# Optimization experiments

Hardware: AMD Instinct MI355X
Metric: run time of the kernel (lower is better)

## Reference

```python
import jax, jax.numpy as jnp
import numpy as np

NUM_HEADS = 16
HIDDEN = 1024
HEAD_DIM = HIDDEN // NUM_HEADS


def setup_inputs() -> dict:
    key = jax.random.key(0)
    ks = jax.random.split(key, 9)
    B, S = 2, 2048
    s = 1.0 / np.sqrt(HIDDEN)
    return {
        "x": jax.random.normal(ks[0], (B, S, HIDDEN), dtype=jnp.float32),
        "Wq": jax.random.normal(ks[1], (HIDDEN, HIDDEN), dtype=jnp.float32) * s,
        "bq": jnp.zeros((HIDDEN,), dtype=jnp.float32),
        "Wk": jax.random.normal(ks[2], (HIDDEN, HIDDEN), dtype=jnp.float32) * s,
        "bk": jnp.zeros((HIDDEN,), dtype=jnp.float32),
        "Wv": jax.random.normal(ks[3], (HIDDEN, HIDDEN), dtype=jnp.float32) * s,
        "bv": jnp.zeros((HIDDEN,), dtype=jnp.float32),
        "Wo": jax.random.normal(ks[4], (HIDDEN, HIDDEN), dtype=jnp.float32) * s,
        "bo": jnp.zeros((HIDDEN,), dtype=jnp.float32),
    }


def reference(x, Wq, bq, Wk, bk, Wv, bv, Wo, bo):
    B, S, H = x.shape
    # project and split heads: [B, S, H] -> [B, nh, S, hd]
    def split_heads(t):
        return t.reshape(B, S, NUM_HEADS, HEAD_DIM).transpose(0, 2, 1, 3)

    q = split_heads(x @ Wq + bq)
    k = split_heads(x @ Wk + bk)
    v = split_heads(x @ Wv + bv)

    scores = jnp.einsum("bhqd,bhkd->bhqk", q, k) / jnp.sqrt(
        jnp.asarray(HEAD_DIM, dtype=x.dtype))
    probs = jax.nn.softmax(scores, axis=-1)
    # attn_drop_rate = 0.0 -> dropout is identity
    ctx = jnp.einsum("bhqk,bhkd->bhqd", probs, v)
    ctx = ctx.transpose(0, 2, 1, 3).reshape(B, S, H)
    out = ctx @ Wo + bo
    return out
```

## Files before the change

kernel.cpp:

```cpp
#include <hip/hip_runtime.h>

#define NHEADS 16
#define HDIM   64
#define SEQL   2048
#define HID    1024
#define NB     2
#define MT     4096

#define QSCALE 0.18033688011112042f

typedef float        f4_t   __attribute__((ext_vector_type(4)));
typedef float        f32x16 __attribute__((ext_vector_type(16)));
typedef unsigned int u32x4  __attribute__((ext_vector_type(4)));
typedef __bf16       bf16x8 __attribute__((ext_vector_type(8)));

typedef const __attribute__((address_space(1))) unsigned int* gas_ptr;
typedef __attribute__((address_space(3))) unsigned int*       las_ptr;

__device__ __forceinline__ void gload16(const void* g, void* l){
  __builtin_amdgcn_global_load_lds((gas_ptr)g, (las_ptr)l, 16, 0, 0);
}
__device__ __forceinline__ unsigned int pkbf(float a, float b){
  unsigned short lo = __builtin_bit_cast(unsigned short, (__bf16)a);
  unsigned short hi = __builtin_bit_cast(unsigned short, (__bf16)b);
  return (unsigned)lo | ((unsigned)hi << 16);
}
__device__ __forceinline__ unsigned short f2bf(float f){
  return __builtin_bit_cast(unsigned short, (__bf16)f);
}
__device__ __forceinline__ u32x4 ld16(const unsigned short* p){
  return *reinterpret_cast<const u32x4*>(p);
}
__device__ __forceinline__ f4_t mfma_bf16(u32x4 a, u32x4 b, f4_t c){
  return __builtin_amdgcn_mfma_f32_16x16x32_bf16(
      __builtin_bit_cast(bf16x8, a), __builtin_bit_cast(bf16x8, b), c, 0, 0, 0);
}
__device__ __forceinline__ f32x16 mfma32(u32x4 a, u32x4 b, f32x16 c){
  return __builtin_amdgcn_mfma_f32_32x32x16_bf16(
      __builtin_bit_cast(bf16x8, a), __builtin_bit_cast(bf16x8, b), c, 0, 0, 0);
}

#if __has_builtin(__builtin_amdgcn_permlane32_swap)
typedef unsigned int u32x2 __attribute__((ext_vector_type(2)));
__device__ __forceinline__ void plswap(unsigned int &a, unsigned int &b){
  u32x2 r = __builtin_amdgcn_permlane32_swap(a, b, false, false);
  a = r[0]; b = r[1];
}
#else
__device__ __forceinline__ void plswap(unsigned int &a, unsigned int &b){
  unsigned int as = (unsigned int)__shfl_xor((int)a, 32);
  unsigned int bs = (unsigned int)__shfl_xor((int)b, 32);
  bool hi = (threadIdx.x & 32) != 0;
  unsigned int na = hi ? bs : a;
  unsigned int nb = hi ? b  : as;
  a = na; b = nb;
}
#endif

__global__ __launch_bounds__(256) void xcast(const float* __restrict__ x,
                                             unsigned short* __restrict__ xb){
  int gid = blockIdx.x * 256 + threadIdx.x;
  float4 a = reinterpret_cast<const float4*>(x)[gid * 2];
  float4 b = reinterpret_cast<const float4*>(x)[gid * 2 + 1];
  u32x4 o;
  o[0] = pkbf(a.x, a.y);
  o[1] = pkbf(a.z, a.w);
  o[2] = pkbf(b.x, b.y);
  o[3] = pkbf(b.z, b.w);
  *reinterpret_cast<u32x4*>(&xb[gid * 8]) = o;
}

__global__ void prep_w(const float* __restrict__ Wq, const float* __restrict__ Wk,
                       const float* __restrict__ Wv, const float* __restrict__ Wo,
                       unsigned short* __restrict__ wqT, unsigned short* __restrict__ wkT,
                       unsigned short* __restrict__ wvT, unsigned short* __restrict__ woT){
  __shared__ float t[32][33];
  int z = blockIdx.z;
  const float* W = (z==0)?Wq:(z==1)?Wk:(z==2)?Wv:Wo;
  unsigned short* WT = (z==0)?wqT:(z==1)?wkT:(z==2)?wvT:woT;
  float sc = (z==0) ? QSCALE : 1.0f;
  int k0 = blockIdx.x*32, n0 = blockIdx.y*32;
  int tx = threadIdx.x, ty = threadIdx.y;
  #pragma unroll
  for (int ii=0; ii<4; ii++)
    t[ty+ii*8][tx] = W[(k0+ty+ii*8)*HID + n0+tx];
  __syncthreads();
  #pragma unroll
  for (int ii=0; ii<4; ii++)
    WT[(n0+ty+ii*8)*HID + k0+tx] = f2bf(t[tx][ty+ii*8] * sc);
}

__global__ __launch_bounds__(256) void qkv_gemm(
    const unsigned short* __restrict__ xb,
    const unsigned short* __restrict__ wqT, const unsigned short* __restrict__ wkT,
    const unsigned short* __restrict__ wvT,
    const float* __restrict__ bq, const float* __restrict__ bk, const float* __restrict__ bv,
    unsigned short* __restrict__ qo, unsigned short* __restrict__ ko,
    unsigned short* __restrict__ vto){
  __shared__ unsigned short As[2][128*32];
  __shared__ unsigned short Bs[2][128*32];
  const int z = blockIdx.z;
  const unsigned short* wT = (z==0)?wqT:(z==1)?wkT:wvT;
  const float* bias = (z==0)?bq:(z==1)?bk:bv;
  const float bscale = (z==0) ? QSCALE : 1.0f;
  const int m0 = blockIdx.x * 128;
  const int n0 = blockIdx.y * 128;
  const int tid = threadIdx.x;
  const int lane = tid & 63, w = tid >> 6;
  const int l15 = lane & 15, lg = lane >> 4;
  const int wr = (w >> 1) * 64, wc = (w & 1) * 64;
  const int srow = w*16 + (lane >> 2);
  const int skc  = (lane & 3) * 8;

  f4_t acc[4][4];
  f4_t z4 = {0.f, 0.f, 0.f, 0.f};
  #pragma unroll
  for (int i=0;i<4;i++)
    #pragma unroll
    for (int j=0;j<4;j++) acc[i][j] = z4;

  auto stageg = [&](int buf, int kt){
    #pragma unroll
    for (int c = 0; c < 2; c++) {
      int row = c*64 + srow;
      gload16(&xb[(m0+row)*HID + kt + skc], (char*)As[buf] + c*4096 + w*1024);
      gload16(&wT[(n0+row)*HID + kt + skc], (char*)Bs[buf] + c*4096 + w*1024);
    }
  };

  stageg(0, 0);
  int cur = 0;
  for (int kt = 0; kt < HID; kt += 32) {
    __syncthreads();
    if (kt + 32 < HID) stageg(cur^1, kt + 32);
    u32x4 a[4], b[4];
    #pragma unroll
    for (int i=0;i<4;i++) a[i] = ld16(&As[cur][(wr + i*16 + l15)*32 + lg*8]);
    #pragma unroll
    for (int j=0;j<4;j++) b[j] = ld16(&Bs[cur][(wc + j*16 + l15)*32 + lg*8]);
    __builtin_amdgcn_s_setprio(1);
    #pragma unroll
    for (int i=0;i<4;i++)
      #pragma unroll
      for (int j=0;j<4;j++)
        acc[i][j] = mfma_bf16(a[i], b[j], acc[i][j]);
    __builtin_amdgcn_s_setprio(0);
    cur ^= 1;
  }
  if (z == 2) {
    #pragma unroll
    for (int i=0;i<4;i++){
      int mrow = m0 + wr + i*16 + lg*4;
      int b_ = mrow >> 11, s = mrow & 2047;
      #pragma unroll
      for (int j=0;j<4;j++){
        int n = n0 + wc + j*16 + l15;
        float bs = bias[n];
        int h = n >> 6, d = n & 63;
        unsigned int lo = pkbf(acc[i][j][0]+bs, acc[i][j][1]+bs);
        unsigned int hi = pkbf(acc[i][j][2]+bs, acc[i][j][3]+bs);
        unsigned long long v8 = (unsigned long long)lo | ((unsigned long long)hi << 32);
        *reinterpret_cast<unsigned long long*>(
            vto + (((b_*NHEADS + h)*HDIM + d)*SEQL + s)) = v8;
      }
    }
  } else {
    unsigned short* outp = (z==0) ? qo : ko;
    #pragma unroll
    for (int i=0;i<4;i++){
      int mrow = m0 + wr + i*16 + lg*4;
      #pragma unroll
      for (int j=0;j<4;j++){
        int n = n0 + wc + j*16 + l15;
        float bs = bias[n] * bscale;
        int h = n >> 6, d = n & 63;
        #pragma unroll
        for (int r=0;r<4;r++){
          int m = mrow + r;
          int b_ = m >> 11, s = m & 2047;
          outp[(((b_*NHEADS + h)*SEQL) + s)*HDIM + d] = f2bf(acc[i][j][r] + bs);
        }
      }
    }
  }
}

__global__ __launch_bounds__(256, 4) void flash(
    const unsigned short* __restrict__ q,
    const unsigned short* __restrict__ k,
    const unsigned short* __restrict__ vT,
    float* __restrict__ po,
    float* __restrict__ pl,
    int kspan){
  __shared__ unsigned short Ks[2][4096];
  __shared__ unsigned short Vs[2][4096];
  const int bh = blockIdx.y;
  const int z = blockIdx.z;
  const int kb0 = z * kspan;
  const int tid = threadIdx.x;
  const int w = tid >> 6, lane = tid & 63;
  const int l31 = lane & 31, hi = lane >> 5;
  const int q0 = blockIdx.x*128 + w*32;
  const unsigned short* qb = q + (bh*SEQL + q0)*HDIM;
  const unsigned short* kp = k + bh*SEQL*HDIM;
  const unsigned short* vp = vT + bh*HDIM*SEQL;

  const int sr = w*16 + (lane >> 3);
  const int scol = ((lane & 7) ^ (sr & 7)) * 8;
  const int ldst = w*2048;

  u32x4 qf[4];
  #pragma unroll
  for (int c=0;c<4;c++)
    qf[c] = ld16(&qb[l31*HDIM + c*16 + hi*8]);

  u32x4 ones;
  ones[0] = 0x3F803F80u; ones[1] = 0x3F803F80u;
  ones[2] = 0x3F803F80u; ones[3] = 0x3F803F80u;

  f32x16 oacc[2], lsacc;
  f32x16 z16 = {0.f,0.f,0.f,0.f,0.f,0.f,0.f,0.f,0.f,0.f,0.f,0.f,0.f,0.f,0.f,0.f};
  oacc[0] = z16; oacc[1] = z16; lsacc = z16;

  auto stage = [&](int buf, int kb){
    const unsigned short* gk = kp + (kb + sr)*HDIM + scol;
    gload16(gk,          (char*)Ks[buf] + ldst);
    gload16(gk + 8*HDIM, (char*)Ks[buf] + ldst + 1024);
    const unsigned short* gv = vp + sr*SEQL + kb + scol;
    gload16(gv,          (char*)Vs[buf] + ldst);
    gload16(gv + 8*SEQL, (char*)Vs[buf] + ldst + 1024);
  };

  int cur = 0;
  stage(0, kb0);
  __syncthreads();

  const int rs = (l31 & 7) << 4;

  for (int kb = kb0; kb < kb0 + kspan; kb += 64) {
    if (kb + 64 < kb0 + kspan) stage(cur^1, kb + 64);
    const char* kbase = (const char*)Ks[cur];
    const char* vbase = (const char*)Vs[cur];

    f32x16 sacc[2];
    __builtin_amdgcn_s_setprio(1);
    #pragma unroll
    for (int t=0;t<2;t++){
      const char* rowb = kbase + (t*32 + l31)*128;
      #pragma unroll
      for (int c=0;c<4;c++){
        u32x4 kf = *reinterpret_cast<const u32x4*>(rowb + ((c*32 + hi*16) ^ rs));
        sacc[t] = (c==0) ? mfma32(kf, qf[0], z16) : mfma32(kf, qf[c], sacc[t]);
      }
    }
    __builtin_amdgcn_s_setprio(0);

    #pragma unroll
    for (int t=0;t<2;t++)
      #pragma unroll
      for (int r=0;r<16;r++) sacc[t][r] = exp2f(sacc[t][r]);

    u32x4 pa[4];
    #pragma unroll
    for (int t=0;t<2;t++)
      #pragma unroll
      for (int hf=0;hf<2;hf++){
        unsigned int c1 = pkbf(sacc[t][hf*8+0], sacc[t][hf*8+1]);
        unsigned int c2 = pkbf(sacc[t][hf*8+2], sacc[t][hf*8+3]);
        unsigned int c3 = pkbf(sacc[t][hf*8+4], sacc[t][hf*8+5]);
        unsigned int c4 = pkbf(sacc[t][hf*8+6], sacc[t][hf*8+7]);
        plswap(c1, c3);
        plswap(c2, c4);
        u32x4 f; f[0]=c1; f[1]=c2; f[2]=c3; f[3]=c4;
        pa[t*2+hf] = f;
      }

    __builtin_amdgcn_s_setprio(1);
    #pragma unroll
    for (int dt=0;dt<2;dt++){
      const char* rowb = vbase + (dt*32 + l31)*128;
      #pragma unroll
      for (int ks=0;ks<4;ks++){
        u32x4 vf = *reinterpret_cast<const u32x4*>(rowb + ((ks*32 + hi*16) ^ rs));
        oacc[dt] = mfma32(vf, pa[ks], oacc[dt]);
      }
    }
    #pragma unroll
    for (int ks=0;ks<4;ks++)
      lsacc = mfma32(ones, pa[ks], lsacc);
    __builtin_amdgcn_s_setprio(0);
    __syncthreads();
    cur ^= 1;
  }

  const int rowi = (z*NB*NHEADS + bh)*SEQL + q0 + l31;
  #pragma unroll
  for (int dt=0;dt<2;dt++){
    #pragma unroll
    for (int kq=0;kq<4;kq++){
      float4 o4;
      o4.x = oacc[dt][kq*4+0]; o4.y = oacc[dt][kq*4+1];
      o4.z = oacc[dt][kq*4+2]; o4.w = oacc[dt][kq*4+3];
      *reinterpret_cast<float4*>(po + rowi*HDIM + dt*32 + kq*8 + hi*4) = o4;
    }
  }
  if (hi == 0) pl[rowi] = lsacc[0];
}

__global__ __launch_bounds__(256) void combine(
    const float* __restrict__ po, const float* __restrict__ pl,
    unsigned short* __restrict__ ctx, int nsplit){
  int i = blockIdx.x*256 + threadIdx.x;
  int dq = i & 15;
  int rsi = i >> 4;
  int bh = rsi >> 11, s = rsi & 2047;
  int b_ = bh >> 4, h = bh & 15;
  float L = pl[rsi];
  float4 acc = reinterpret_cast<const float4*>(po)[rsi*16 + dq];
  for (int sp = 1; sp < nsplit; sp++) {
    float4 o1 = reinterpret_cast<const float4*>(po)[rsi*16 + dq + sp*NB*NHEADS*SEQL*16];
    L += pl[rsi + sp*NB*NHEADS*SEQL];
    acc.x += o1.x; acc.y += o1.y; acc.z += o1.z; acc.w += o1.w;
  }
  float inv = 1.0f / L;
  unsigned int lo = pkbf(acc.x*inv, acc.y*inv);
  unsigned int hv = pkbf(acc.z*inv, acc.w*inv);
  unsigned long long v8 = (unsigned long long)lo | ((unsigned long long)hv << 32);
  *reinterpret_cast<unsigned long long*>(
      ctx + (b_*SEQL + s)*HID + h*HDIM + dq*4) = v8;
}

__global__ __launch_bounds__(256) void out_gemm(
    const unsigned short* __restrict__ cb,
    const unsigned short* __restrict__ woT,
    const float* __restrict__ bo,
    float* __restrict__ out){
  __shared__ unsigned short As[2][128*32];
  __shared__ unsigned short Bs[2][128*32];
  const int m0 = blockIdx.x * 128;
  const int n0 = blockIdx.y * 128;
  const int tid = threadIdx.x;
  const int lane = tid & 63, w = tid >> 6;
  const int l15 = lane & 15, lg = lane >> 4;
  const int wr = (w >> 1) * 64, wc = (w & 1) * 64;
  const int srow = w*16 + (lane >> 2);
  const int skc  = (lane & 3) * 8;

  f4_t acc[4][4];
  f4_t z4 = {0.f,0.f,0.f,0.f};
  #pragma unroll
  for (int i=0;i<4;i++)
    #pragma unroll
    for (int j=0;j<4;j++) acc[i][j] = z4;

  auto stageg = [&](int buf, int kt){
    #pragma unroll
    for (int c = 0; c < 2; c++) {
      int row = c*64 + srow;
      gload16(&cb[(m0+row)*HID + kt + skc],  (char*)As[buf] + c*4096 + w*1024);
      gload16(&woT[(n0+row)*HID + kt + skc], (char*)Bs[buf] + c*4096 + w*1024);
    }
  };

  stageg(0, 0);
  int cur = 0;
  for (int kt = 0; kt < HID; kt += 32) {
    __syncthreads();
    if (kt + 32 < HID) stageg(cur^1, kt + 32);
    u32x4 a[4], b[4];
    #pragma unroll
    for (int i=0;i<4;i++) a[i] = ld16(&As[cur][(wr + i*16 + l15)*32 + lg*8]);
    #pragma unroll
    for (int j=0;j<4;j++) b[j] = ld16(&Bs[cur][(wc + j*16 + l15)*32 + lg*8]);
    __builtin_amdgcn_s_setprio(1);
    #pragma unroll
    for (int i=0;i<4;i++)
      #pragma unroll
      for (int j=0;j<4;j++)
        acc[i][j] = mfma_bf16(a[i], b[j], acc[i][j]);
    __builtin_amdgcn_s_setprio(0);
    cur ^= 1;
  }
  #pragma unroll
  for (int i=0;i<4;i++){
    int mrow = m0 + wr + i*16 + lg*4;
    #pragma unroll
    for (int j=0;j<4;j++){
      int n = n0 + wc + j*16 + l15;
      float bs = bo[n];
      #pragma unroll
      for (int r=0;r<4;r++)
        out[(mrow + r)*HID + n] = acc[i][j][r] + bs;
    }
  }
}

extern "C" void kernel_launch(void* const* d_in, const int* in_sizes, int n_in,
                              void* d_out, int out_size, void* d_ws, size_t ws_size,
                              hipStream_t stream){
  const float* x  = (const float*)d_in[0];
  const float* Wq = (const float*)d_in[1];
  const float* bq = (const float*)d_in[2];
  const float* Wk = (const float*)d_in[3];
  const float* bk = (const float*)d_in[4];
  const float* Wv = (const float*)d_in[5];
  const float* bv = (const float*)d_in[6];
  const float* Wo = (const float*)d_in[7];
  const float* bo = (const float*)d_in[8];
  float* out = (float*)d_out;

  char* ws = (char*)d_ws;
  size_t off = 0;
  auto alloc = [&](size_t bytes) -> void* {
    void* p = ws + off;
    off += (bytes + 255) & ~(size_t)255;
    return p;
  };
  unsigned short* xb   = (unsigned short*)alloc((size_t)MT*HID*2);
  unsigned short* wqT  = (unsigned short*)alloc((size_t)HID*HID*2);
  unsigned short* wkT  = (unsigned short*)alloc((size_t)HID*HID*2);
  unsigned short* wvT  = (unsigned short*)alloc((size_t)HID*HID*2);
  unsigned short* woT  = (unsigned short*)alloc((size_t)HID*HID*2);
  unsigned short* q_ws = (unsigned short*)alloc((size_t)MT*HID*2);
  unsigned short* k_ws = (unsigned short*)alloc((size_t)MT*HID*2);
  unsigned short* vT_ws= (unsigned short*)alloc((size_t)MT*HID*2);
  unsigned short* c_ws = (unsigned short*)alloc((size_t)MT*HID*2);
  size_t base_off = off;

  int nsplit = 1;
  {
    size_t need4 = base_off + (((size_t)4*MT*HID*4 + 255) & ~(size_t)255)
                            + (((size_t)4*NB*NHEADS*SEQL*4 + 255) & ~(size_t)255);
    size_t need2 = base_off + (((size_t)2*MT*HID*4 + 255) & ~(size_t)255)
                            + (((size_t)2*NB*NHEADS*SEQL*4 + 255) & ~(size_t)255);
    if (ws_size >= need4) nsplit = 4;
    else if (ws_size >= need2) nsplit = 2;
  }
  float* po = (float*)alloc((size_t)nsplit*MT*HID*4);
  float* pl = (float*)alloc((size_t)nsplit*NB*NHEADS*SEQL*4);
  int kspan = SEQL / nsplit;

  prep_w<<<dim3(32,32,4), dim3(32,8), 0, stream>>>(Wq,Wk,Wv,Wo, wqT,wkT,wvT,woT);
  xcast<<<dim3(2048), dim3(256), 0, stream>>>(x, xb);
  qkv_gemm<<<dim3(32,8,3), dim3(256), 0, stream>>>(xb, wqT,wkT,wvT, bq,bk,bv,
                                                   q_ws, k_ws, vT_ws);
  flash<<<dim3(16,32,nsplit), dim3(256), 0, stream>>>(q_ws, k_ws, vT_ws,
                                                      po, pl, kspan);
  combine<<<dim3(MT*HID/4/256), dim3(256), 0, stream>>>(po, pl, c_ws, nsplit);
  out_gemm<<<dim3(32,8), dim3(256), 0, stream>>>(c_ws, woT, bo, out);
}
```

Measured before the change: 158.1 us.

## Software-pipeline flash loop so PV of previous tile overlaps QK and exp

Restructures the flash attention inner loop into a two-tile unrolled software pipeline. Each half loads V fragments into registers, computes QK for the current tile, runs the PV MFMAs of the previous tile, then does exp and packing, so matrix work overlaps the transcendental work. It also drops the occupancy hint from launch bounds to allow more registers, and caps the KV split at 2 instead of 4. The trade-off is higher register pressure, lower occupancy and fewer flash blocks, which may hurt latency hiding. The loop also assumes an even iteration count.

```diff
diff --git a/kernel.cpp b/kernel.cpp
--- a/kernel.cpp
+++ b/kernel.cpp
@@ -185,7 +185,7 @@
   }
 }
 
-__global__ __launch_bounds__(256, 4) void flash(
+__global__ __launch_bounds__(256) void flash(
     const unsigned short* __restrict__ q,
     const unsigned short* __restrict__ k,
     const unsigned short* __restrict__ vT,
@@ -231,19 +231,17 @@
     gload16(gv + 8*SEQL, (char*)Vs[buf] + ldst + 1024);
   };
 
-  int cur = 0;
-  stage(0, kb0);
-  __syncthreads();
-
   const int rs = (l31 & 7) << 4;
 
-  for (int kb = kb0; kb < kb0 + kspan; kb += 64) {
-    if (kb + 64 < kb0 + kspan) stage(cur^1, kb + 64);
-    const char* kbase = (const char*)Ks[cur];
-    const char* vbase = (const char*)Vs[cur];
-
-    f32x16 sacc[2];
-    __builtin_amdgcn_s_setprio(1);
+  auto loadV = [&](u32x4* vf, const char* vbase){
+    #pragma unroll
+    for (int dt=0;dt<2;dt++)
+      #pragma unroll
+      for (int ks=0;ks<4;ks++)
+        vf[dt*4+ks] = *reinterpret_cast<const u32x4*>(
+            vbase + (dt*32 + l31)*128 + ((ks*32 + hi*16) ^ rs));
+  };
+  auto qk = [&](f32x16* sacc, const char* kbase){
     #pragma unroll
     for (int t=0;t<2;t++){
       const char* rowb = kbase + (t*32 + l31)*128;
@@ -253,14 +251,24 @@
         sacc[t] = (c==0) ? mfma32(kf, qf[0], z16) : mfma32(kf, qf[c], sacc[t]);
       }
     }
+  };
+  auto pv = [&](const u32x4* vf, const u32x4* pa){
+    __builtin_amdgcn_s_setprio(1);
+    #pragma unroll
+    for (int dt=0;dt<2;dt++)
+      #pragma unroll
+      for (int ks=0;ks<4;ks++)
+        oacc[dt] = mfma32(vf[dt*4+ks], pa[ks], oacc[dt]);
+    #pragma unroll
+    for (int ks=0;ks<4;ks++)
+      lsacc = mfma32(ones, pa[ks], lsacc);
     __builtin_amdgcn_s_setprio(0);
-
+  };
+  auto exppack = [&](f32x16* sacc, u32x4* pa){
     #pragma unroll
     for (int t=0;t<2;t++)
       #pragma unroll
       for (int r=0;r<16;r++) sacc[t][r] = exp2f(sacc[t][r]);
-
-    u32x4 pa[4];
     #pragma unroll
     for (int t=0;t<2;t++)
       #pragma unroll
@@ -274,24 +282,31 @@
         u32x4 f; f[0]=c1; f[1]=c2; f[2]=c3; f[3]=c4;
         pa[t*2+hf] = f;
       }
-
-    __builtin_amdgcn_s_setprio(1);
-    #pragma unroll
-    for (int dt=0;dt<2;dt++){
-      const char* rowb = vbase + (dt*32 + l31)*128;
-      #pragma unroll
-      for (int ks=0;ks<4;ks++){
-        u32x4 vf = *reinterpret_cast<const u32x4*>(rowb + ((ks*32 + hi*16) ^ rs));
-        oacc[dt] = mfma32(vf, pa[ks], oacc[dt]);
-      }
-    }
-    #pragma unroll
-    for (int ks=0;ks<4;ks++)
-      lsacc = mfma32(ones, pa[ks], lsacc);
-    __builtin_amdgcn_s_setprio(0);
+  };
+
+  u32x4 vfA[8], vfB[8], paA[4], paB[4];
+
+  stage(0, kb0);
+  __syncthreads();
+
+  const int niter = kspan >> 6;
+  for (int it = 0; it < niter; it += 2) {
+    int kb = kb0 + it*64;
+    if (it + 1 < niter) stage(1, kb + 64);
+    f32x16 sacc[2];
+    loadV(vfA, (const char*)Vs[0]);
+    qk(sacc, (const char*)Ks[0]);
+    if (it > 0) pv(vfB, paB);
+    exppack(sacc, paA);
     __syncthreads();
-    cur ^= 1;
-  }
+    if (it + 2 < niter) stage(0, kb + 128);
+    loadV(vfB, (const char*)Vs[1]);
+    qk(sacc, (const char*)Ks[1]);
+    pv(vfA, paA);
+    exppack(sacc, paB);
+    __syncthreads();
+  }
+  pv(vfB, paB);
 
   const int rowi = (z*NB*NHEADS + bh)*SEQL + q0 + l31;
   #pragma unroll
@@ -429,12 +444,9 @@
 
   int nsplit = 1;
   {
-    size_t need4 = base_off + (((size_t)4*MT*HID*4 + 255) & ~(size_t)255)
-                            + (((size_t)4*NB*NHEADS*SEQL*4 + 255) & ~(size_t)255);
     size_t need2 = base_off + (((size_t)2*MT*HID*4 + 255) & ~(size_t)255)
                             + (((size_t)2*NB*NHEADS*SEQL*4 + 255) & ~(size_t)255);
-    if (ws_size >= need4) nsplit = 4;
-    else if (ws_size >= need2) nsplit = 2;
+    if (ws_size >= need2) nsplit = 2;
   }
   float* po = (float*)alloc((size_t)nsplit*MT*HID*4);
   float* pl = (float*)alloc((size_t)nsplit*NB*NHEADS*SEQL*4);
```

Result: no change. 156.3 us (-1.2%).

## Fuse split-KV combine into output projection GEMM A-tile loading

Applied to the files above, without the earlier changes.

Removes the separate combine kernel and its bf16 context buffer. The output GEMM now reads the fp32 partial outputs and log-sum values directly, sums the splits, normalizes, converts to bf16 and writes the A tile to shared memory through registers, overlapped with the MFMA loop. It also caps nsplit at 2, dropping the 4-way split option. This saves one launch and a round trip through memory, but each output-GEMM block re-reads the fp32 partials eight times (once per N block), and the flash kernel may now run with less parallelism.

```diff
diff --git a/kernel.cpp b/kernel.cpp
--- a/kernel.cpp
+++ b/kernel.cpp
@@ -307,34 +307,11 @@
   if (hi == 0) pl[rowi] = lsacc[0];
 }
 
-__global__ __launch_bounds__(256) void combine(
+__global__ __launch_bounds__(256) void out_gemm(
     const float* __restrict__ po, const float* __restrict__ pl,
-    unsigned short* __restrict__ ctx, int nsplit){
-  int i = blockIdx.x*256 + threadIdx.x;
-  int dq = i & 15;
-  int rsi = i >> 4;
-  int bh = rsi >> 11, s = rsi & 2047;
-  int b_ = bh >> 4, h = bh & 15;
-  float L = pl[rsi];
-  float4 acc = reinterpret_cast<const float4*>(po)[rsi*16 + dq];
-  for (int sp = 1; sp < nsplit; sp++) {
-    float4 o1 = reinterpret_cast<const float4*>(po)[rsi*16 + dq + sp*NB*NHEADS*SEQL*16];
-    L += pl[rsi + sp*NB*NHEADS*SEQL];
-    acc.x += o1.x; acc.y += o1.y; acc.z += o1.z; acc.w += o1.w;
-  }
-  float inv = 1.0f / L;
-  unsigned int lo = pkbf(acc.x*inv, acc.y*inv);
-  unsigned int hv = pkbf(acc.z*inv, acc.w*inv);
-  unsigned long long v8 = (unsigned long long)lo | ((unsigned long long)hv << 32);
-  *reinterpret_cast<unsigned long long*>(
-      ctx + (b_*SEQL + s)*HID + h*HDIM + dq*4) = v8;
-}
-
-__global__ __launch_bounds__(256) void out_gemm(
-    const unsigned short* __restrict__ cb,
     const unsigned short* __restrict__ woT,
     const float* __restrict__ bo,
-    float* __restrict__ out){
+    float* __restrict__ out, int nsplit){
   __shared__ unsigned short As[2][128*32];
   __shared__ unsigned short Bs[2][128*32];
   const int m0 = blockIdx.x * 128;
@@ -345,6 +322,7 @@
   const int wr = (w >> 1) * 64, wc = (w & 1) * 64;
   const int srow = w*16 + (lane >> 2);
   const int skc  = (lane & 3) * 8;
+  const int spo = NB*NHEADS*SEQL;
 
   f4_t acc[4][4];
   f4_t z4 = {0.f,0.f,0.f,0.f};
@@ -353,20 +331,65 @@
     #pragma unroll
     for (int j=0;j<4;j++) acc[i][j] = z4;
 
-  auto stageg = [&](int buf, int kt){
-    #pragma unroll
-    for (int c = 0; c < 2; c++) {
+  float4 areg[2][4];
+  float  Lreg[2];
+
+  auto loadA = [&](int kt){
+    int h = kt >> 6;
+    int d0 = (kt & 63) + skc;
+    #pragma unroll
+    for (int c=0;c<2;c++){
+      int m = m0 + c*64 + srow;
+      int b_ = m >> 11, s = m & 2047;
+      int ri = (b_*NHEADS + h)*SEQL + s;
+      const float* p0 = po + (size_t)ri*HDIM + d0;
+      areg[c][0] = *reinterpret_cast<const float4*>(p0);
+      areg[c][1] = *reinterpret_cast<const float4*>(p0 + 4);
+      float L = pl[ri];
+      if (nsplit == 2){
+        const float* p1 = p0 + (size_t)spo*HDIM;
+        areg[c][2] = *reinterpret_cast<const float4*>(p1);
+        areg[c][3] = *reinterpret_cast<const float4*>(p1 + 4);
+        L += pl[ri + spo];
+      }
+      Lreg[c] = L;
+    }
+  };
+  auto writeA = [&](int buf){
+    #pragma unroll
+    for (int c=0;c<2;c++){
+      float4 lo = areg[c][0], hi = areg[c][1];
+      if (nsplit == 2){
+        lo.x += areg[c][2].x; lo.y += areg[c][2].y;
+        lo.z += areg[c][2].z; lo.w += areg[c][2].w;
+        hi.x += areg[c][3].x; hi.y += areg[c][3].y;
+        hi.z += areg[c][3].z; hi.w += areg[c][3].w;
+      }
+      float inv = 1.0f / Lreg[c];
+      u32x4 o;
+      o[0] = pkbf(lo.x*inv, lo.y*inv);
+      o[1] = pkbf(lo.z*inv, lo.w*inv);
+      o[2] = pkbf(hi.x*inv, hi.y*inv);
+      o[3] = pkbf(hi.z*inv, hi.w*inv);
+      *reinterpret_cast<u32x4*>(&As[buf][(c*64 + srow)*32 + skc]) = o;
+    }
+  };
+  auto stageB = [&](int buf, int kt){
+    #pragma unroll
+    for (int c=0;c<2;c++){
       int row = c*64 + srow;
-      gload16(&cb[(m0+row)*HID + kt + skc],  (char*)As[buf] + c*4096 + w*1024);
       gload16(&woT[(n0+row)*HID + kt + skc], (char*)Bs[buf] + c*4096 + w*1024);
     }
   };
 
-  stageg(0, 0);
+  loadA(0);
+  stageB(0, 0);
+  writeA(0);
   int cur = 0;
   for (int kt = 0; kt < HID; kt += 32) {
     __syncthreads();
-    if (kt + 32 < HID) stageg(cur^1, kt + 32);
+    bool nxt = (kt + 32 < HID);
+    if (nxt) { loadA(kt + 32); stageB(cur^1, kt + 32); }
     u32x4 a[4], b[4];
     #pragma unroll
     for (int i=0;i<4;i++) a[i] = ld16(&As[cur][(wr + i*16 + l15)*32 + lg*8]);
@@ -379,6 +402,7 @@
       for (int j=0;j<4;j++)
         acc[i][j] = mfma_bf16(a[i], b[j], acc[i][j]);
     __builtin_amdgcn_s_setprio(0);
+    if (nxt) writeA(cur^1);
     cur ^= 1;
   }
   #pragma unroll
@@ -424,17 +448,13 @@
   unsigned short* q_ws = (unsigned short*)alloc((size_t)MT*HID*2);
   unsigned short* k_ws = (unsigned short*)alloc((size_t)MT*HID*2);
   unsigned short* vT_ws= (unsigned short*)alloc((size_t)MT*HID*2);
-  unsigned short* c_ws = (unsigned short*)alloc((size_t)MT*HID*2);
   size_t base_off = off;
 
   int nsplit = 1;
   {
-    size_t need4 = base_off + (((size_t)4*MT*HID*4 + 255) & ~(size_t)255)
-                            + (((size_t)4*NB*NHEADS*SEQL*4 + 255) & ~(size_t)255);
     size_t need2 = base_off + (((size_t)2*MT*HID*4 + 255) & ~(size_t)255)
                             + (((size_t)2*NB*NHEADS*SEQL*4 + 255) & ~(size_t)255);
-    if (ws_size >= need4) nsplit = 4;
-    else if (ws_size >= need2) nsplit = 2;
+    if (ws_size >= need2) nsplit = 2;
   }
   float* po = (float*)alloc((size_t)nsplit*MT*HID*4);
   float* pl = (float*)alloc((size_t)nsplit*NB*NHEADS*SEQL*4);
@@ -446,6 +466,5 @@
                                                    q_ws, k_ws, vT_ws);
   flash<<<dim3(16,32,nsplit), dim3(256), 0, stream>>>(q_ws, k_ws, vT_ws,
                                                       po, pl, kspan);
-  combine<<<dim3(MT*HID/4/256), dim3(256), 0, stream>>>(po, pl, c_ws, nsplit);
-  out_gemm<<<dim3(32,8), dim3(256), 0, stream>>>(c_ws, woT, bo, out);
-}
+  out_gemm<<<dim3(32,8), dim3(256), 0, stream>>>(po, pl, woT, bo, out, nsplit);
+}
```

Result: slower. 177.4 us (+12.2%).
